# Kernel tuning notes

Hardware: AMD Instinct MI355X
Metric: run time of the kernel (lower is better)

The kernel has to match this reference:

```python
import jax, jax.numpy as jnp
import numpy as np

ALPHA = 0.2  # leaky relu slope
NEG = -9e15  # mask fill value from the torch code


def gat_layer(x, adj_mask, W, a):
    """One dense GAT attention head.
    Equivalent math to the torch layer, without materializing the
    [N, N, 2F] a_input tensor: a^T [h_i ; h_j] = (h @ a1)_i + (h @ a2)_j.
    x: [N, Fin], adj_mask: [N, N] bool, W: [Fin, Fout], a: [2*Fout, 1].
    """
    h = x @ W                              # [N, Fout]
    Fo = W.shape[1]
    s_src = h @ a[:Fo, 0]                  # [N]
    s_dst = h @ a[Fo:, 0]                  # [N]
    e = jax.nn.leaky_relu(s_src[:, None] + s_dst[None, :], ALPHA)  # [N, N]
    e = jnp.where(adj_mask, e, NEG)
    attn = jax.nn.softmax(e, axis=1)       # dropout is a no-op in eval mode
    return attn @ h                        # [N, Fout]


def setup_inputs() -> dict:
    key = jax.random.key(0)
    ks = jax.random.split(key, 6)
    N, nfeat, nhid, nclass, nheads = 4096, 512, 64, 32, 8
    x = jax.random.normal(ks[0], (N, nfeat), dtype=jnp.float32)
    adj = jax.random.randint(ks[1], (N, N), 0, 2, dtype=jnp.int32)
    # params scaled like torch uniform(-1/sqrt(fan_in), 1/sqrt(fan_in))
    W_att = jax.random.normal(ks[2], (nheads, nfeat, nhid), dtype=jnp.float32) / np.sqrt(nfeat)
    a_att = jax.random.normal(ks[3], (nheads, 2 * nhid, 1), dtype=jnp.float32) / np.sqrt(2 * nhid)
    W_out = jax.random.normal(ks[4], (nhid * nheads, nclass), dtype=jnp.float32) / np.sqrt(nhid * nheads)
    a_out = jax.random.normal(ks[5], (2 * nclass, 1), dtype=jnp.float32) / np.sqrt(2 * nclass)
    return {"x": x, "adj": adj, "W_att": W_att, "a_att": a_att,
            "W_out": W_out, "a_out": a_out}


def reference(x, adj, W_att, a_att, W_out, a_out):
    adj_mask = adj > 0  # [N, N]
    # multi-head layer, concat=True => elu per head, concat along features
    heads = jax.vmap(lambda W, a: jax.nn.elu(gat_layer(x, adj_mask, W, a)))(W_att, a_att)  # [H, N, nhid]
    H, N, Fh = heads.shape
    hcat = jnp.transpose(heads, (1, 0, 2)).reshape(N, H * Fh)  # [N, H*nhid]
    # output layer, concat=False, then elu applied by GAT.forward
    out = jax.nn.elu(gat_layer(hcat, adj_mask, W_out, a_out))  # [N, nclass]
    return out
```

## Files before the change

kernel.cpp:

```cpp
#include <hip/hip_runtime.h>
#include <math.h>

#define NN 4096
#define CC 512
#define MB (1024*1024)
#define LOG2E 1.4426950408889634f

typedef __attribute__((ext_vector_type(8))) __bf16 bf16x8;
typedef __attribute__((ext_vector_type(4))) float f32x4;
typedef unsigned short ushort_t;
typedef unsigned int uint_t;
typedef unsigned char uchar_t;

#if __has_builtin(__builtin_amdgcn_exp2f)
#define EXP2(x) __builtin_amdgcn_exp2f(x)
#else
#define EXP2(x) exp2f(x)
#endif

static __device__ __forceinline__ float elu1(float x){ return x > 0.f ? x : (__expf(x)-1.f); }
static __device__ __forceinline__ ushort_t f2bf(float f){
    union { float f; uint_t u; } v; v.f = f;
    uint_t r = (v.u + 0x7FFFu + ((v.u >> 16) & 1u)) >> 16;
    return (ushort_t)r;
}

__global__ void k_repack(const float* __restrict__ Watt, float* __restrict__ Wall){
    int idx = blockIdx.x*256 + threadIdx.x;
    int k = idx >> 9, c = idx & 511;
    Wall[idx] = Watt[(c>>6)*(512*64) + k*64 + (c&63)];
}

__global__ void k_pack(const int* __restrict__ adj, uint_t* __restrict__ abits){
    int idx = blockIdx.x*256 + threadIdx.x;
    int i = idx >> 7, q = idx & 127;
    const int4* p = (const int4*)&adj[(size_t)i*NN + q*32];
    uint_t m = 0;
    #pragma unroll
    for(int g=0; g<8; g++){
        int4 v = p[g];
        m |= (uint_t)(v.x > 0) << (g*4 + 0);
        m |= (uint_t)(v.y > 0) << (g*4 + 1);
        m |= (uint_t)(v.z > 0) << (g*4 + 2);
        m |= (uint_t)(v.w > 0) << (g*4 + 3);
    }
    abits[idx] = m;
}

template<int BN, int TN>
__global__ __launch_bounds__(256) void k_gemm(const float* __restrict__ A,
                                              const float* __restrict__ B,
                                              float* __restrict__ C,
                                              int M, int N, int K){
    constexpr int BM = 64, BK = 16, TM = 4;
    __shared__ float As[BK][BM + 4];
    __shared__ float Bs[BK][BN];
    const int t = threadIdx.x;
    const int i0 = blockIdx.x*BM, j0 = blockIdx.y*BN;
    constexpr int nx = BN / TN;
    const int ty = t / nx, tx = t % nx;
    float acc[TM][TN];
    #pragma unroll
    for(int a=0;a<TM;a++){
        #pragma unroll
        for(int b=0;b<TN;b++) acc[a][b] = 0.f;
    }
    const int ai = t >> 2, ak = (t & 3)*4;
    for(int k0 = 0; k0 < K; k0 += BK){
        __syncthreads();
        float4 av = *(const float4*)&A[(size_t)(i0+ai)*K + k0 + ak];
        As[ak+0][ai]=av.x; As[ak+1][ai]=av.y; As[ak+2][ai]=av.z; As[ak+3][ai]=av.w;
        if constexpr (BN == 64){
            int bk = t >> 4, bj = (t & 15)*4;
            *(float4*)&Bs[bk][bj] = *(const float4*)&B[(size_t)(k0+bk)*N + j0 + bj];
        } else {
            if (t < 128){
                int bk = t >> 3, bj = (t & 7)*4;
                *(float4*)&Bs[bk][bj] = *(const float4*)&B[(size_t)(k0+bk)*N + j0 + bj];
            }
        }
        __syncthreads();
        #pragma unroll
        for(int k=0;k<BK;k++){
            float4 a4 = *(const float4*)&As[k][ty*TM];
            float ar[4] = {a4.x, a4.y, a4.z, a4.w};
            if constexpr (TN == 4){
                float4 b4 = *(const float4*)&Bs[k][tx*4];
                float br[4] = {b4.x, b4.y, b4.z, b4.w};
                #pragma unroll
                for(int a=0;a<TM;a++){
                    #pragma unroll
                    for(int b=0;b<4;b++) acc[a][b] += ar[a]*br[b];
                }
            } else {
                float2 b2 = *(const float2*)&Bs[k][tx*2];
                #pragma unroll
                for(int a=0;a<TM;a++){ acc[a][0] += ar[a]*b2.x; acc[a][1] += ar[a]*b2.y; }
            }
        }
    }
    #pragma unroll
    for(int a=0;a<TM;a++){
        float* cp = &C[(size_t)(i0 + ty*TM + a)*N + j0 + tx*TN];
        if constexpr (TN == 4){
            float4 v = {acc[a][0], acc[a][1], acc[a][2], acc[a][3]};
            *(float4*)cp = v;
        } else {
            float2 v = {acc[a][0], acc[a][1]};
            *(float2*)cp = v;
        }
    }
}

__global__ __launch_bounds__(256) void k_tr(const float* __restrict__ h, ushort_t* __restrict__ hT){
    __shared__ float tile[32][33];
    const int bj = blockIdx.x*32, bc = blockIdx.y*32;
    const int tx = threadIdx.x & 31, ty = threadIdx.x >> 5;
    #pragma unroll
    for(int r=0;r<4;r++)
        tile[ty + r*8][tx] = h[(size_t)(bj + ty + r*8)*512 + bc + tx];
    __syncthreads();
    #pragma unroll
    for(int r=0;r<4;r++)
        hT[(size_t)(bc + ty + r*8)*NN + bj + tx] = f2bf(tile[tx][ty + r*8]);
}

__global__ void k_scores1(const float* __restrict__ hall, const float* __restrict__ aatt,
                          float* __restrict__ ssrc2, float* __restrict__ sdst2){
    int t = threadIdx.x;
    int hd = t & 7, il = t >> 3;
    int i = blockIdx.x*32 + il;
    const float4* h4 = (const float4*)&hall[(size_t)i*CC + hd*64];
    const float4* a1 = (const float4*)&aatt[hd*128];
    const float4* a2 = (const float4*)&aatt[hd*128 + 64];
    float ss = 0.f, sd = 0.f;
    #pragma unroll
    for(int q=0;q<16;q++){
        float4 h = h4[q], u = a1[q], v = a2[q];
        ss += h.x*u.x + h.y*u.y + h.z*u.z + h.w*u.w;
        sd += h.x*v.x + h.y*v.y + h.z*v.z + h.w*v.w;
    }
    ssrc2[hd*NN + i] = ss*LOG2E;
    sdst2[hd*NN + i] = sd*LOG2E;
}

__global__ __launch_bounds__(256) void k_attn1(
        const ushort_t* __restrict__ hT,
        const float* __restrict__ ssrc2, const float* __restrict__ sdst2,
        const uchar_t* __restrict__ abits,
        float* __restrict__ pnumT, float* __restrict__ pden){
    const int t = threadIdx.x;
    const int l = t & 63;
    const int hd0 = (t >> 6)*2;
    const int i0 = blockIdx.x*32;
    const int jc = blockIdx.y;
    const int lr = l & 15;
    const int lg = l >> 4;

    f32x4 acc[2][2][4] = {};
    f32x4 dacc[2][2] = {};

    float ss[2][2];
    #pragma unroll
    for(int hd=0;hd<2;hd++)
        #pragma unroll
        for(int mh=0;mh<2;mh++)
            ss[hd][mh] = ssrc2[(hd0+hd)*NN + i0 + mh*16 + lr];

    bf16x8 ones;
    #pragma unroll
    for(int e=0;e<8;e++) ones[e] = (__bf16)1.0f;

    const uchar_t* arow0 = &abits[(size_t)(i0 + lr)*512 + jc*128];
    const uchar_t* arow1 = &abits[(size_t)(i0 + 16 + lr)*512 + jc*128];

    bf16x8 bA[2][4], bB[2][4];
    float4 sdaA[2], sdbA[2], sdaB[2], sdbB[2];
    uint_t bitsA0, bitsA1, bitsB0, bitsB1;

#define LOAD1(SFX, JT) { \
    const int jb_ = jc*1024 + (JT)*32 + lg*8; \
    _Pragma("unroll") \
    for(int hd=0;hd<2;hd++){ \
        _Pragma("unroll") \
        for(int nt=0;nt<4;nt++) \
            b##SFX[hd][nt] = *(const bf16x8*)&hT[(size_t)((hd0+hd)*64 + nt*16 + lr)*NN + jb_]; \
        sda##SFX[hd] = *(const float4*)&sdst2[(hd0+hd)*NN + jb_]; \
        sdb##SFX[hd] = *(const float4*)&sdst2[(hd0+hd)*NN + jb_ + 4]; \
    } \
    bits##SFX##0 = arow0[(JT)*4 + lg]; \
    bits##SFX##1 = arow1[(JT)*4 + lg]; }

#define COMP1(SFX) { \
    _Pragma("unroll") \
    for(int hd=0;hd<2;hd++){ \
        float sdv[8] = {sda##SFX[hd].x, sda##SFX[hd].y, sda##SFX[hd].z, sda##SFX[hd].w, \
                        sdb##SFX[hd].x, sdb##SFX[hd].y, sdb##SFX[hd].z, sdb##SFX[hd].w}; \
        _Pragma("unroll") \
        for(int mh=0;mh<2;mh++){ \
            const uint_t bits = mh ? bits##SFX##1 : bits##SFX##0; \
            bf16x8 a; \
            _Pragma("unroll") \
            for(int e=0;e<8;e++){ \
                float s_ = ss[hd][mh] + sdv[e]; \
                float t_ = fmaxf(s_, 0.2f*s_); \
                float w_ = EXP2(t_) * (float)((bits >> e) & 1u); \
                a[e] = (__bf16)w_; \
            } \
            _Pragma("unroll") \
            for(int nt=0;nt<4;nt++) \
                acc[hd][mh][nt] = __builtin_amdgcn_mfma_f32_16x16x32_bf16( \
                    a, b##SFX[hd][nt], acc[hd][mh][nt], 0, 0, 0); \
            dacc[hd][mh] = __builtin_amdgcn_mfma_f32_16x16x32_bf16( \
                    a, ones, dacc[hd][mh], 0, 0, 0); \
        } \
    } }

    LOAD1(A, 0);
    for(int jt=0; jt<32; jt+=2){
        LOAD1(B, jt+1);
        COMP1(A);
        if (jt + 2 < 32) LOAD1(A, jt+2);
        COMP1(B);
    }
#undef LOAD1
#undef COMP1

    #pragma unroll
    for(int hd=0;hd<2;hd++)
        #pragma unroll
        for(int mh=0;mh<2;mh++)
            #pragma unroll
            for(int nt=0;nt<4;nt++){
                int col = (hd0+hd)*64 + nt*16 + lr;
                float4 v = {acc[hd][mh][nt][0], acc[hd][mh][nt][1],
                            acc[hd][mh][nt][2], acc[hd][mh][nt][3]};
                *(float4*)&pnumT[((size_t)jc*512 + col)*NN + i0 + mh*16 + lg*4] = v;
            }
    if (lr == 0){
        #pragma unroll
        for(int hd=0;hd<2;hd++)
            #pragma unroll
            for(int mh=0;mh<2;mh++)
                #pragma unroll
                for(int r=0;r<4;r++)
                    pden[((size_t)jc*8 + hd0+hd)*NN + i0 + mh*16 + lg*4 + r] = dacc[hd][mh][r];
    }
}

__global__ void k_reduce1T(const float* __restrict__ pnumT, const float* __restrict__ pden,
                           float* __restrict__ hcatT){
    int idx = blockIdx.x*256 + threadIdx.x;
    int c = idx >> 12, i = idx & 4095, hd = c >> 6;
    float s = 0.f, d = 0.f;
    #pragma unroll
    for(int jc=0;jc<4;jc++){
        s += pnumT[((size_t)jc*512 + c)*NN + i];
        d += pden[((size_t)jc*8 + hd)*NN + i];
    }
    hcatT[(size_t)c*NN + i] = elu1(s/d);
}

__global__ __launch_bounds__(256) void k_gemmAT(const float* __restrict__ AT,
                                                const float* __restrict__ B,
                                                float* __restrict__ C){
    __shared__ float As[32][32];
    __shared__ float Bs[32][32];
    const int t = threadIdx.x;
    const int i0 = blockIdx.x*32;
    const int ty = t >> 4, tx = t & 15;
    float acc[2][2] = {{0.f,0.f},{0.f,0.f}};
    for(int k0=0;k0<512;k0+=32){
        __syncthreads();
        { int k = t >> 3, i4 = (t & 7)*4;
          *(float4*)&As[k][i4] = *(const float4*)&AT[(size_t)(k0+k)*NN + i0 + i4]; }
        { int k = t >> 3, n4 = (t & 7)*4;
          *(float4*)&Bs[k][n4] = *(const float4*)&B[(size_t)(k0+k)*32 + n4]; }
        __syncthreads();
        #pragma unroll
        for(int k=0;k<32;k++){
            float2 a2 = *(const float2*)&As[k][ty*2];
            float2 b2 = *(const float2*)&Bs[k][tx*2];
            acc[0][0] += a2.x*b2.x; acc[0][1] += a2.x*b2.y;
            acc[1][0] += a2.y*b2.x; acc[1][1] += a2.y*b2.y;
        }
    }
    #pragma unroll
    for(int a=0;a<2;a++){
        float2 v = {acc[a][0], acc[a][1]};
        *(float2*)&C[(size_t)(i0 + ty*2 + a)*32 + tx*2] = v;
    }
}

__global__ void k_scores2(const float* __restrict__ h2, const float* __restrict__ aout,
                          float* __restrict__ ss2, float* __restrict__ sd2){
    int i = blockIdx.x*256 + threadIdx.x;
    const float4* h4 = (const float4*)&h2[(size_t)i*32];
    const float4* a1 = (const float4*)aout;
    const float4* a2 = (const float4*)&aout[32];
    float ss = 0.f, sd = 0.f;
    #pragma unroll
    for(int q=0;q<8;q++){
        float4 h = h4[q], u = a1[q], v = a2[q];
        ss += h.x*u.x + h.y*u.y + h.z*u.z + h.w*u.w;
        sd += h.x*v.x + h.y*v.y + h.z*v.z + h.w*v.w;
    }
    ss2[i] = ss*LOG2E; sd2[i] = sd*LOG2E;
}

__global__ __launch_bounds__(256) void k_tr2(const float* __restrict__ h2, ushort_t* __restrict__ h2T){
    __shared__ float tile[64][33];
    const int bj = blockIdx.x*64;
    const int t = threadIdx.x;
    const int tx = t & 31, ty = t >> 5;
    #pragma unroll
    for(int r=0;r<8;r++)
        tile[ty + r*8][tx] = h2[(size_t)(bj + ty + r*8)*32 + tx];
    __syncthreads();
    #pragma unroll
    for(int half=0; half<2; half++){
        int c = (t >> 4) + half*16;
        int j4 = (t & 15)*4;
        ushort4 o;
        o.x = f2bf(tile[j4+0][c]); o.y = f2bf(tile[j4+1][c]);
        o.z = f2bf(tile[j4+2][c]); o.w = f2bf(tile[j4+3][c]);
        *(ushort4*)&h2T[(size_t)c*NN + bj + j4] = o;
    }
}

__global__ __launch_bounds__(256) void k_attn2(
        const ushort_t* __restrict__ h2T,
        const float* __restrict__ ss2, const float* __restrict__ sd2,
        const uchar_t* __restrict__ abits,
        float* __restrict__ pnum2T, float* __restrict__ pden2){
    const int t = threadIdx.x;
    const int l = t & 63;
    const int wv = t >> 6;
    const int i0 = blockIdx.x*16;
    const int jc = blockIdx.y;
    const int lr = l & 15, lg = l >> 4;
    const int jcw = jc*4 + wv;

    f32x4 acc[2] = {};
    f32x4 dacc = {};
    const float ss = ss2[i0 + lr];
    bf16x8 ones;
    #pragma unroll
    for(int e=0;e<8;e++) ones[e] = (__bf16)1.0f;

    const uchar_t* arow = &abits[(size_t)(i0+lr)*512 + jc*128 + wv*4];

    bf16x8 bA[2], bB[2];
    float4 sdaA, sdbA, sdaB, sdbB;
    uint_t bitsA, bitsB;

#define LOAD2(SFX, JT) { \
    const int jb_ = jc*1024 + (JT)*128 + wv*32 + lg*8; \
    _Pragma("unroll") \
    for(int nt=0;nt<2;nt++) \
        b##SFX[nt] = *(const bf16x8*)&h2T[(size_t)(nt*16 + lr)*NN + jb_]; \
    sda##SFX = *(const float4*)&sd2[jb_]; \
    sdb##SFX = *(const float4*)&sd2[jb_ + 4]; \
    bits##SFX = arow[(JT)*16 + lg]; }

#define COMP2(SFX) { \
    float sdv[8] = {sda##SFX.x, sda##SFX.y, sda##SFX.z, sda##SFX.w, \
                    sdb##SFX.x, sdb##SFX.y, sdb##SFX.z, sdb##SFX.w}; \
    bf16x8 a; \
    _Pragma("unroll") \
    for(int e=0;e<8;e++){ \
        float s_ = ss + sdv[e]; \
        float t_ = fmaxf(s_, 0.2f*s_); \
        float w_ = EXP2(t_) * (float)((bits##SFX >> e) & 1u); \
        a[e] = (__bf16)w_; \
    } \
    _Pragma("unroll") \
    for(int nt=0;nt<2;nt++) \
        acc[nt] = __builtin_amdgcn_mfma_f32_16x16x32_bf16(a, b##SFX[nt], acc[nt], 0, 0, 0); \
    dacc = __builtin_amdgcn_mfma_f32_16x16x32_bf16(a, ones, dacc, 0, 0, 0); }

    LOAD2(A, 0);
    for(int jt=0; jt<8; jt+=2){
        LOAD2(B, jt+1);
        COMP2(A);
        if (jt + 2 < 8) LOAD2(A, jt+2);
        COMP2(B);
    }
#undef LOAD2
#undef COMP2

    #pragma unroll
    for(int nt=0;nt<2;nt++){
        int col = nt*16 + lr;
        float4 v = {acc[nt][0], acc[nt][1], acc[nt][2], acc[nt][3]};
        *(float4*)&pnum2T[((size_t)jcw*32 + col)*NN + i0 + lg*4] = v;
    }
    if (lr == 0){
        #pragma unroll
        for(int r=0;r<4;r++)
            pden2[(size_t)jcw*NN + i0 + lg*4 + r] = dacc[r];
    }
}

__global__ void k_reduce2(const float* __restrict__ pnum2T, const float* __restrict__ pden2,
                          float* __restrict__ out){
    int idx = blockIdx.x*256 + threadIdx.x;
    int c = idx >> 12, i = idx & 4095;
    float s = 0.f, d = 0.f;
    #pragma unroll
    for(int jcw=0;jcw<16;jcw++){
        s += pnum2T[((size_t)jcw*32 + c)*NN + i];
        d += pden2[(size_t)jcw*NN + i];
    }
    out[(size_t)i*32 + c] = elu1(s/d);
}

extern "C" void kernel_launch(void* const* d_in, const int* in_sizes, int n_in,
                              void* d_out, int out_size, void* d_ws, size_t ws_size,
                              hipStream_t stream){
    const float* x    = (const float*)d_in[0];
    const int*   adj  = (const int*)  d_in[1];
    const float* Watt = (const float*)d_in[2];
    const float* aatt = (const float*)d_in[3];
    const float* Wout = (const float*)d_in[4];
    const float* aout = (const float*)d_in[5];
    float* out = (float*)d_out;
    char* ws = (char*)d_ws;

    float*    h_all = (float*)   (ws + (size_t) 0*MB);
    float*    hcatT = (float*)   (ws + (size_t) 0*MB);
    float*    W_all = (float*)   (ws + (size_t) 8*MB);
    float*    ssrc2 = (float*)   (ws + (size_t) 9*MB);
    float*    sdst2 = (float*)   (ws + (size_t)10*MB);
    ushort_t* hT    = (ushort_t*)(ws + (size_t)11*MB);
    uint_t*   abits = (uint_t*)  (ws + (size_t)15*MB);
    float*    h2    = (float*)   (ws + (size_t)17*MB);
    float*    ss2   = (float*)   (ws + (size_t)18*MB);
    float*    sd2   = (float*)   (ws + (size_t)19*MB);
    ushort_t* h2T   = (ushort_t*)(ws + (size_t)20*MB);
    float*    pden  = (float*)   (ws + (size_t)21*MB);
    float*    pden2 = (float*)   (ws + (size_t)21*MB + 512*1024);
    float*    pnumT = (float*)   (ws + (size_t)22*MB);
    float*    pnum2T= pnumT;
    if (ws_size < (size_t)55*MB) return;

    k_repack  <<<1024, 256, 0, stream>>>(Watt, W_all);
    k_pack    <<<2048, 256, 0, stream>>>(adj, abits);
    k_gemm<64,4><<<dim3(64,8), 256, 0, stream>>>(x, W_all, h_all, NN, 512, 512);
    k_tr      <<<dim3(128,16), 256, 0, stream>>>(h_all, hT);
    k_scores1 <<<128, 256, 0, stream>>>(h_all, aatt, ssrc2, sdst2);
    k_attn1   <<<dim3(128,4), 256, 0, stream>>>(hT, ssrc2, sdst2, (const uchar_t*)abits, pnumT, pden);
    k_reduce1T<<<8192, 256, 0, stream>>>(pnumT, pden, hcatT);
    k_gemmAT  <<<128, 256, 0, stream>>>(hcatT, Wout, h2);
    k_scores2 <<<16, 256, 0, stream>>>(h2, aout, ss2, sd2);
    k_tr2     <<<64, 256, 0, stream>>>(h2, h2T);
    k_attn2   <<<dim3(256,4), 256, 0, stream>>>(h2T, ss2, sd2, (const uchar_t*)abits, pnum2T, pden2);
    k_reduce2 <<<512, 256, 0, stream>>>(pnum2T, pden2, out);
}
```

Baseline: 288.6 us.

## Use split-bf16 MFMA for first GEMM, fuse transposes and scores, rebalance attention

The first projection GEMM moves from scalar FP32 to bf16 MFMA, using a hi/lo split (three MFMAs per tile) to keep near-FP32 accuracy. It writes both h_all and the bf16 transposed hT, which removes the separate transpose kernel. The second GEMM now also emits bf16 h2T and computes the output-layer scores with wavefront shuffles, replacing two small kernels. The first attention kernel gives each head pair its own block and splits the j range across waves, reducing partials through shared memory to halve the reduce work. The cost is extra prep kernels that write split copies of x and W, plus more shared-memory synchronisation.

Measured after the change: 299.4 us. +3.7%, slower.

```diff
diff --git a/kernel.cpp b/kernel.cpp
--- a/kernel.cpp
+++ b/kernel.cpp
@@ -24,11 +24,36 @@
     uint_t r = (v.u + 0x7FFFu + ((v.u >> 16) & 1u)) >> 16;
     return (ushort_t)r;
 }
-
-__global__ void k_repack(const float* __restrict__ Watt, float* __restrict__ Wall){
+static __device__ __forceinline__ float bf2f(ushort_t h){
+    union { uint_t u; float f; } q; q.u = ((uint_t)h) << 16; return q.f;
+}
+
+__global__ void k_prepW(const float* __restrict__ Watt,
+                        ushort_t* __restrict__ Wh, ushort_t* __restrict__ Wl){
     int idx = blockIdx.x*256 + threadIdx.x;
-    int k = idx >> 9, c = idx & 511;
-    Wall[idx] = Watt[(c>>6)*(512*64) + k*64 + (c&63)];
+    int c = idx >> 7, kq = idx & 127, k = kq*4;
+    ushort4 h4, l4;
+    float v[4];
+    #pragma unroll
+    for(int j=0;j<4;j++)
+        v[j] = Watt[(c>>6)*(512*64) + (k+j)*64 + (c&63)];
+    h4.x = f2bf(v[0]); h4.y = f2bf(v[1]); h4.z = f2bf(v[2]); h4.w = f2bf(v[3]);
+    l4.x = f2bf(v[0]-bf2f(h4.x)); l4.y = f2bf(v[1]-bf2f(h4.y));
+    l4.z = f2bf(v[2]-bf2f(h4.z)); l4.w = f2bf(v[3]-bf2f(h4.w));
+    *(ushort4*)&Wh[(size_t)c*512 + k] = h4;
+    *(ushort4*)&Wl[(size_t)c*512 + k] = l4;
+}
+
+__global__ void k_splitx(const float* __restrict__ x,
+                         ushort_t* __restrict__ xh, ushort_t* __restrict__ xl){
+    int idx = blockIdx.x*256 + threadIdx.x;
+    float4 v = *(const float4*)&x[(size_t)idx*4];
+    ushort4 h4, l4;
+    h4.x = f2bf(v.x); h4.y = f2bf(v.y); h4.z = f2bf(v.z); h4.w = f2bf(v.w);
+    l4.x = f2bf(v.x-bf2f(h4.x)); l4.y = f2bf(v.y-bf2f(h4.y));
+    l4.z = f2bf(v.z-bf2f(h4.z)); l4.w = f2bf(v.w-bf2f(h4.w));
+    *(ushort4*)&xh[(size_t)idx*4] = h4;
+    *(ushort4*)&xl[(size_t)idx*4] = l4;
 }
 
 __global__ void k_pack(const int* __restrict__ adj, uint_t* __restrict__ abits){
@@ -47,82 +72,46 @@
     abits[idx] = m;
 }
 
-template<int BN, int TN>
-__global__ __launch_bounds__(256) void k_gemm(const float* __restrict__ A,
-                                              const float* __restrict__ B,
-                                              float* __restrict__ C,
-                                              int M, int N, int K){
-    constexpr int BM = 64, BK = 16, TM = 4;
-    __shared__ float As[BK][BM + 4];
-    __shared__ float Bs[BK][BN];
+__global__ __launch_bounds__(256) void k_gemm1(
+        const ushort_t* __restrict__ xh, const ushort_t* __restrict__ xl,
+        const ushort_t* __restrict__ Wh, const ushort_t* __restrict__ Wl,
+        float* __restrict__ h_all, ushort_t* __restrict__ hT){
     const int t = threadIdx.x;
-    const int i0 = blockIdx.x*BM, j0 = blockIdx.y*BN;
-    constexpr int nx = BN / TN;
-    const int ty = t / nx, tx = t % nx;
-    float acc[TM][TN];
-    #pragma unroll
-    for(int a=0;a<TM;a++){
-        #pragma unroll
-        for(int b=0;b<TN;b++) acc[a][b] = 0.f;
-    }
-    const int ai = t >> 2, ak = (t & 3)*4;
-    for(int k0 = 0; k0 < K; k0 += BK){
-        __syncthreads();
-        float4 av = *(const float4*)&A[(size_t)(i0+ai)*K + k0 + ak];
-        As[ak+0][ai]=av.x; As[ak+1][ai]=av.y; As[ak+2][ai]=av.z; As[ak+3][ai]=av.w;
-        if constexpr (BN == 64){
-            int bk = t >> 4, bj = (t & 15)*4;
-            *(float4*)&Bs[bk][bj] = *(const float4*)&B[(size_t)(k0+bk)*N + j0 + bj];
-        } else {
-            if (t < 128){
-                int bk = t >> 3, bj = (t & 7)*4;
-                *(float4*)&Bs[bk][bj] = *(const float4*)&B[(size_t)(k0+bk)*N + j0 + bj];
-            }
+    const int l = t & 63, wv = t >> 6;
+    const int lr = l & 15, lg = l >> 4;
+    const int ib = blockIdx.x*64 + wv*16;
+    const int j0 = blockIdx.y*64;
+
+    f32x4 acc[4] = {};
+    #pragma unroll 2
+    for(int ks=0; ks<16; ks++){
+        const int kb = ks*32 + lg*8;
+        bf16x8 ah = *(const bf16x8*)&xh[(size_t)(ib+lr)*512 + kb];
+        bf16x8 al = *(const bf16x8*)&xl[(size_t)(ib+lr)*512 + kb];
+        bf16x8 bh[4], bl[4];
+        #pragma unroll
+        for(int nt=0;nt<4;nt++){
+            bh[nt] = *(const bf16x8*)&Wh[(size_t)(j0+nt*16+lr)*512 + kb];
+            bl[nt] = *(const bf16x8*)&Wl[(size_t)(j0+nt*16+lr)*512 + kb];
         }
-        __syncthreads();
-        #pragma unroll
-        for(int k=0;k<BK;k++){
-            float4 a4 = *(const float4*)&As[k][ty*TM];
-            float ar[4] = {a4.x, a4.y, a4.z, a4.w};
-            if constexpr (TN == 4){
-                float4 b4 = *(const float4*)&Bs[k][tx*4];
-                float br[4] = {b4.x, b4.y, b4.z, b4.w};
-                #pragma unroll
-                for(int a=0;a<TM;a++){
-                    #pragma unroll
-                    for(int b=0;b<4;b++) acc[a][b] += ar[a]*br[b];
-                }
-            } else {
-                float2 b2 = *(const float2*)&Bs[k][tx*2];
-                #pragma unroll
-                for(int a=0;a<TM;a++){ acc[a][0] += ar[a]*b2.x; acc[a][1] += ar[a]*b2.y; }
-            }
+        #pragma unroll
+        for(int nt=0;nt<4;nt++){
+            acc[nt] = __builtin_amdgcn_mfma_f32_16x16x32_bf16(ah, bh[nt], acc[nt], 0,0,0);
+            acc[nt] = __builtin_amdgcn_mfma_f32_16x16x32_bf16(al, bh[nt], acc[nt], 0,0,0);
+            acc[nt] = __builtin_amdgcn_mfma_f32_16x16x32_bf16(ah, bl[nt], acc[nt], 0,0,0);
         }
     }
     #pragma unroll
-    for(int a=0;a<TM;a++){
-        float* cp = &C[(size_t)(i0 + ty*TM + a)*N + j0 + tx*TN];
-        if constexpr (TN == 4){
-            float4 v = {acc[a][0], acc[a][1], acc[a][2], acc[a][3]};
-            *(float4*)cp = v;
-        } else {
-            float2 v = {acc[a][0], acc[a][1]};
-            *(float2*)cp = v;
-        }
-    }
-}
-
-__global__ __launch_bounds__(256) void k_tr(const float* __restrict__ h, ushort_t* __restrict__ hT){
-    __shared__ float tile[32][33];
-    const int bj = blockIdx.x*32, bc = blockIdx.y*32;
-    const int tx = threadIdx.x & 31, ty = threadIdx.x >> 5;
-    #pragma unroll
-    for(int r=0;r<4;r++)
-        tile[ty + r*8][tx] = h[(size_t)(bj + ty + r*8)*512 + bc + tx];
-    __syncthreads();
-    #pragma unroll
-    for(int r=0;r<4;r++)
-        hT[(size_t)(bc + ty + r*8)*NN + bj + tx] = f2bf(tile[tx][ty + r*8]);
+    for(int nt=0;nt<4;nt++){
+        const int col = j0 + nt*16 + lr;
+        #pragma unroll
+        for(int r=0;r<4;r++)
+            h_all[(size_t)(ib + lg*4 + r)*512 + col] = acc[nt][r];
+        ushort4 o;
+        o.x = f2bf(acc[nt][0]); o.y = f2bf(acc[nt][1]);
+        o.z = f2bf(acc[nt][2]); o.w = f2bf(acc[nt][3]);
+        *(ushort4*)&hT[(size_t)col*NN + ib + lg*4] = o;
+    }
 }
 
 __global__ void k_scores1(const float* __restrict__ hall, const float* __restrict__ aatt,
@@ -150,12 +139,11 @@
         const uchar_t* __restrict__ abits,
         float* __restrict__ pnumT, float* __restrict__ pden){
     const int t = threadIdx.x;
-    const int l = t & 63;
-    const int hd0 = (t >> 6)*2;
+    const int l = t & 63, wv = t >> 6;
+    const int hd0 = blockIdx.z*2;
     const int i0 = blockIdx.x*32;
-    const int jc = blockIdx.y;
-    const int lr = l & 15;
-    const int lg = l >> 4;
+    const int jcc = blockIdx.y;
+    const int lr = l & 15, lg = l >> 4;
 
     f32x4 acc[2][2][4] = {};
     f32x4 dacc[2][2] = {};
@@ -171,15 +159,16 @@
     #pragma unroll
     for(int e=0;e<8;e++) ones[e] = (__bf16)1.0f;
 
-    const uchar_t* arow0 = &abits[(size_t)(i0 + lr)*512 + jc*128];
-    const uchar_t* arow1 = &abits[(size_t)(i0 + 16 + lr)*512 + jc*128];
+    const int jwb = jcc*2048 + wv*512;
+    const uchar_t* arow0 = &abits[(size_t)(i0 + lr)*512 + jcc*256 + wv*64];
+    const uchar_t* arow1 = &abits[(size_t)(i0 + 16 + lr)*512 + jcc*256 + wv*64];
 
     bf16x8 bA[2][4], bB[2][4];
     float4 sdaA[2], sdbA[2], sdaB[2], sdbB[2];
     uint_t bitsA0, bitsA1, bitsB0, bitsB1;
 
 #define LOAD1(SFX, JT) { \
-    const int jb_ = jc*1024 + (JT)*32 + lg*8; \
+    const int jb_ = jwb + (JT)*32 + lg*8; \
     _Pragma("unroll") \
     for(int hd=0;hd<2;hd++){ \
         _Pragma("unroll") \
@@ -217,34 +206,69 @@
     } }
 
     LOAD1(A, 0);
-    for(int jt=0; jt<32; jt+=2){
+    for(int jt=0; jt<16; jt+=2){
         LOAD1(B, jt+1);
         COMP1(A);
-        if (jt + 2 < 32) LOAD1(A, jt+2);
+        if (jt + 2 < 16) LOAD1(A, jt+2);
         COMP1(B);
     }
 #undef LOAD1
 #undef COMP1
 
-    #pragma unroll
-    for(int hd=0;hd<2;hd++)
-        #pragma unroll
-        for(int mh=0;mh<2;mh++)
-            #pragma unroll
-            for(int nt=0;nt<4;nt++){
-                int col = (hd0+hd)*64 + nt*16 + lr;
-                float4 v = {acc[hd][mh][nt][0], acc[hd][mh][nt][1],
-                            acc[hd][mh][nt][2], acc[hd][mh][nt][3]};
-                *(float4*)&pnumT[((size_t)jc*512 + col)*NN + i0 + mh*16 + lg*4] = v;
-            }
-    if (lr == 0){
+    __shared__ f32x4 red[2][20][64];
+    __syncthreads();
+    if (wv >= 2){
         #pragma unroll
         for(int hd=0;hd<2;hd++)
             #pragma unroll
-            for(int mh=0;mh<2;mh++)
+            for(int mh=0;mh<2;mh++){
                 #pragma unroll
-                for(int r=0;r<4;r++)
-                    pden[((size_t)jc*8 + hd0+hd)*NN + i0 + mh*16 + lg*4 + r] = dacc[hd][mh][r];
+                for(int nt=0;nt<4;nt++) red[wv-2][(hd*2+mh)*4+nt][l] = acc[hd][mh][nt];
+                red[wv-2][16 + hd*2+mh][l] = dacc[hd][mh];
+            }
+    }
+    __syncthreads();
+    if (wv < 2){
+        #pragma unroll
+        for(int hd=0;hd<2;hd++)
+            #pragma unroll
+            for(int mh=0;mh<2;mh++){
+                #pragma unroll
+                for(int nt=0;nt<4;nt++) acc[hd][mh][nt] += red[wv][(hd*2+mh)*4+nt][l];
+                dacc[hd][mh] += red[wv][16 + hd*2+mh][l];
+            }
+    }
+    __syncthreads();
+    if (wv == 1){
+        #pragma unroll
+        for(int hd=0;hd<2;hd++)
+            #pragma unroll
+            for(int mh=0;mh<2;mh++){
+                #pragma unroll
+                for(int nt=0;nt<4;nt++) red[0][(hd*2+mh)*4+nt][l] = acc[hd][mh][nt];
+                red[0][16 + hd*2+mh][l] = dacc[hd][mh];
+            }
+    }
+    __syncthreads();
+    if (wv == 0){
+        #pragma unroll
+        for(int hd=0;hd<2;hd++)
+            #pragma unroll
+            for(int mh=0;mh<2;mh++){
+                #pragma unroll
+                for(int nt=0;nt<4;nt++){
+                    f32x4 v = acc[hd][mh][nt] + red[0][(hd*2+mh)*4+nt][l];
+                    int col = (hd0+hd)*64 + nt*16 + lr;
+                    float4 o = {v[0], v[1], v[2], v[3]};
+                    *(float4*)&pnumT[((size_t)jcc*512 + col)*NN + i0 + mh*16 + lg*4] = o;
+                }
+                f32x4 d = dacc[hd][mh] + red[0][16 + hd*2+mh][l];
+                if (lr == 0){
+                    #pragma unroll
+                    for(int r=0;r<4;r++)
+                        pden[((size_t)jcc*8 + hd0+hd)*NN + i0 + mh*16 + lg*4 + r] = d[r];
+                }
+            }
     }
 }
 
@@ -254,16 +278,19 @@
     int c = idx >> 12, i = idx & 4095, hd = c >> 6;
     float s = 0.f, d = 0.f;
     #pragma unroll
-    for(int jc=0;jc<4;jc++){
+    for(int jc=0;jc<2;jc++){
         s += pnumT[((size_t)jc*512 + c)*NN + i];
         d += pden[((size_t)jc*8 + hd)*NN + i];
     }
     hcatT[(size_t)c*NN + i] = elu1(s/d);
 }
 
-__global__ __launch_bounds__(256) void k_gemmAT(const float* __restrict__ AT,
-                                                const float* __restrict__ B,
-                                                float* __restrict__ C){
+__global__ __launch_bounds__(256) void k_gemm2(const float* __restrict__ AT,
+                                               const float* __restrict__ B,
+                                               const float* __restrict__ aout,
+                                               ushort_t* __restrict__ h2T,
+                                               float* __restrict__ ss2,
+                                               float* __restrict__ sd2){
     __shared__ float As[32][32];
     __shared__ float Bs[32][32];
     const int t = threadIdx.x;
@@ -287,44 +314,25 @@
     }
     #pragma unroll
     for(int a=0;a<2;a++){
-        float2 v = {acc[a][0], acc[a][1]};
-        *(float2*)&C[(size_t)(i0 + ty*2 + a)*32 + tx*2] = v;
-    }
-}
-
-__global__ void k_scores2(const float* __restrict__ h2, const float* __restrict__ aout,
-                          float* __restrict__ ss2, float* __restrict__ sd2){
-    int i = blockIdx.x*256 + threadIdx.x;
-    const float4* h4 = (const float4*)&h2[(size_t)i*32];
-    const float4* a1 = (const float4*)aout;
-    const float4* a2 = (const float4*)&aout[32];
-    float ss = 0.f, sd = 0.f;
-    #pragma unroll
-    for(int q=0;q<8;q++){
-        float4 h = h4[q], u = a1[q], v = a2[q];
-        ss += h.x*u.x + h.y*u.y + h.z*u.z + h.w*u.w;
-        sd += h.x*v.x + h.y*v.y + h.z*v.z + h.w*v.w;
-    }
-    ss2[i] = ss*LOG2E; sd2[i] = sd*LOG2E;
-}
-
-__global__ __launch_bounds__(256) void k_tr2(const float* __restrict__ h2, ushort_t* __restrict__ h2T){
-    __shared__ float tile[64][33];
-    const int bj = blockIdx.x*64;
-    const int t = threadIdx.x;
-    const int tx = t & 31, ty = t >> 5;
-    #pragma unroll
-    for(int r=0;r<8;r++)
-        tile[ty + r*8][tx] = h2[(size_t)(bj + ty + r*8)*32 + tx];
-    __syncthreads();
-    #pragma unroll
-    for(int half=0; half<2; half++){
-        int c = (t >> 4) + half*16;
-        int j4 = (t & 15)*4;
-        ushort4 o;
-        o.x = f2bf(tile[j4+0][c]); o.y = f2bf(tile[j4+1][c]);
-        o.z = f2bf(tile[j4+2][c]); o.w = f2bf(tile[j4+3][c]);
-        *(ushort4*)&h2T[(size_t)c*NN + bj + j4] = o;
+        #pragma unroll
+        for(int b=0;b<2;b++)
+            h2T[(size_t)(tx*2+b)*NN + i0 + ty*2 + a] = f2bf(acc[a][b]);
+    }
+    float a1x = aout[tx*2], a1y = aout[tx*2+1];
+    float a2x = aout[32+tx*2], a2y = aout[32+tx*2+1];
+    #pragma unroll
+    for(int a=0;a<2;a++){
+        float ps = acc[a][0]*a1x + acc[a][1]*a1y;
+        float pd = acc[a][0]*a2x + acc[a][1]*a2y;
+        #pragma unroll
+        for(int m=1;m<16;m<<=1){
+            ps += __shfl_xor(ps, m);
+            pd += __shfl_xor(pd, m);
+        }
+        if (tx == 0){
+            ss2[i0 + ty*2 + a] = ps*LOG2E;
+            sd2[i0 + ty*2 + a] = pd*LOG2E;
+        }
     }
 }
 
@@ -429,12 +437,12 @@
 
     float*    h_all = (float*)   (ws + (size_t) 0*MB);
     float*    hcatT = (float*)   (ws + (size_t) 0*MB);
-    float*    W_all = (float*)   (ws + (size_t) 8*MB);
+    ushort_t* Whi   = (ushort_t*)(ws + (size_t) 8*MB);
+    ushort_t* Wlo   = (ushort_t*)(ws + (size_t) 8*MB + 512*1024);
     float*    ssrc2 = (float*)   (ws + (size_t) 9*MB);
     float*    sdst2 = (float*)   (ws + (size_t)10*MB);
     ushort_t* hT    = (ushort_t*)(ws + (size_t)11*MB);
     uint_t*   abits = (uint_t*)  (ws + (size_t)15*MB);
-    float*    h2    = (float*)   (ws + (size_t)17*MB);
     float*    ss2   = (float*)   (ws + (size_t)18*MB);
     float*    sd2   = (float*)   (ws + (size_t)19*MB);
     ushort_t* h2T   = (ushort_t*)(ws + (size_t)20*MB);
@@ -442,18 +450,18 @@
     float*    pden2 = (float*)   (ws + (size_t)21*MB + 512*1024);
     float*    pnumT = (float*)   (ws + (size_t)22*MB);
     float*    pnum2T= pnumT;
+    ushort_t* xh    = (ushort_t*)(ws + (size_t)38*MB);
+    ushort_t* xl    = (ushort_t*)(ws + (size_t)42*MB);
     if (ws_size < (size_t)55*MB) return;
 
-    k_repack  <<<1024, 256, 0, stream>>>(Watt, W_all);
+    k_prepW   <<<256, 256, 0, stream>>>(Watt, Whi, Wlo);
+    k_splitx  <<<2048, 256, 0, stream>>>(x, xh, xl);
     k_pack    <<<2048, 256, 0, stream>>>(adj, abits);
-    k_gemm<64,4><<<dim3(64,8), 256, 0, stream>>>(x, W_all, h_all, NN, 512, 512);
-    k_tr      <<<dim3(128,16), 256, 0, stream>>>(h_all, hT);
+    k_gemm1   <<<dim3(64,8), 256, 0, stream>>>(xh, xl, Whi, Wlo, h_all, hT);
     k_scores1 <<<128, 256, 0, stream>>>(h_all, aatt, ssrc2, sdst2);
-    k_attn1   <<<dim3(128,4), 256, 0, stream>>>(hT, ssrc2, sdst2, (const uchar_t*)abits, pnumT, pden);
+    k_attn1   <<<dim3(128,2,4), 256, 0, stream>>>(hT, ssrc2, sdst2, (const uchar_t*)abits, pnumT, pden);
     k_reduce1T<<<8192, 256, 0, stream>>>(pnumT, pden, hcatT);
-    k_gemmAT  <<<128, 256, 0, stream>>>(hcatT, Wout, h2);
-    k_scores2 <<<16, 256, 0, stream>>>(h2, aout, ss2, sd2);
-    k_tr2     <<<64, 256, 0, stream>>>(h2, h2T);
+    k_gemm2   <<<128, 256, 0, stream>>>(hcatT, Wout, aout, h2T, ss2, sd2);
     k_attn2   <<<dim3(256,4), 256, 0, stream>>>(h2T, ss2, sd2, (const uchar_t*)abits, pnum2T, pden2);
     k_reduce2 <<<512, 256, 0, stream>>>(pnum2T, pden2, out);
 }
```
